# Kernel tuning notes

Measured on AMD Instinct MI355X. Metric: run time of the kernel, lower is better.

The kernel has to match this reference:

```python
import jax, jax.numpy as jnp
import numpy as np

NUM_EDGE_CLASS = 4
NODE_DIM = 64
BATCH = 32
NUM_NODES = 1024


def setup_inputs() -> dict:
    key = jax.random.key(0)
    k1, k2, k3, k4, k5 = jax.random.split(key, 5)
    node_state = jax.random.normal(k1, (BATCH, NUM_NODES, NODE_DIM), dtype=jnp.float32)
    adj_mat = jax.random.randint(k2, (BATCH, NUM_NODES, NUM_NODES), 0, NUM_EDGE_CLASS, dtype=jnp.int32)
    matrix_in = jax.random.normal(k3, (NUM_EDGE_CLASS, NODE_DIM, NODE_DIM), dtype=jnp.float32) * 0.1
    matrix_out = jax.random.normal(k4, (NUM_EDGE_CLASS, NODE_DIM, NODE_DIM), dtype=jnp.float32) * 0.1
    bias = jax.random.normal(k5, (2 * NODE_DIM,), dtype=jnp.float32)
    return {"node_state": node_state, "adj_mat": adj_mat,
            "matrix_in": matrix_in, "matrix_out": matrix_out, "bias": bias}


def reference(node_state, adj_mat, matrix_in, matrix_out, bias):
    """GGNN message passing (Li et al. Eq. 2).

    Original TF code builds a [b, n*d, n*d] block matrix where block (i, j)
    is matrix_in[adj_mat[b, i, j]] (and matrix_out[adj_mat[b, j, i]] for the
    outgoing direction), then matmuls against flattened node states. The
    equivalent fused math is:
      m_in[b,i]  = sum_j matrix_in[adj[b,i,j]]  @ h[b,j]
      m_out[b,i] = sum_j matrix_out[adj[b,j,i]] @ h[b,j]
    Implemented via a one-hot over the (small) set of edge classes so the
    per-edge d x d matrices are never materialized per edge.
    """
    h = node_state  # [b, n, d]
    onehot = jax.nn.one_hot(adj_mat, NUM_EDGE_CLASS, dtype=h.dtype)  # [b, n, n, c]
    # per-class neighbor aggregation, then one small matmul per class
    s_in = jnp.einsum('bijc,bje->bice', onehot, h)          # [b, n, c, d]
    m_in = jnp.einsum('bice,cde->bid', s_in, matrix_in)      # [b, n, d]
    s_out = jnp.einsum('bjic,bje->bice', onehot, h)          # transposed adjacency
    m_out = jnp.einsum('bice,cde->bid', s_out, matrix_out)   # [b, n, d]
    message = jnp.concatenate([m_in, m_out], axis=-1) + bias  # [b, n, 2d]
    return message
```

## Files before the change

### kernel.cpp

```cpp
#include <hip/hip_runtime.h>


namespace {

typedef unsigned int  u32;
typedef unsigned short u16;
typedef __attribute__((ext_vector_type(8))) short bf16x8;
typedef __attribute__((ext_vector_type(4))) float f32x4;

constexpr int NN = 1024;
constexpr int ND = 64;

__device__ inline u16 f2bf(float x) {
    u32 u = __float_as_uint(x);
    return (u16)((u + 0x7FFFu + ((u >> 16) & 1u)) >> 16);
}
__device__ inline float bf2f(u16 x) { return __uint_as_float(((u32)x) << 16); }

__device__ inline u32 oh2(u32 z) {
    return ((z & 1u) | ((z & 4u) << 14)) * 0x3F80u;
}

__global__ __launch_bounds__(256) void pack_adj(
    const int* __restrict__ adj, u32* __restrict__ adjP, u32* __restrict__ adjPT)
{
    __shared__ u32 rp[64][16];
    const int t = threadIdx.x;
    const int bid = blockIdx.x;
    const int b = bid >> 6, It = (bid >> 4) & 3, Jt = (bid >> 2) & 3, s = bid & 3;
    const int* base = adj + ((size_t)b << 20) + (size_t)(It * 256 + s * 64) * NN + Jt * 256;

    const int row = t >> 2, seg = t & 3;
    const int* rptr = base + (size_t)row * NN + seg * 64;
    u32 w[4];
    #pragma unroll
    for (int q = 0; q < 4; ++q) {
        int4 v0 = *(const int4*)(rptr + q * 16 + 0);
        int4 v1 = *(const int4*)(rptr + q * 16 + 4);
        int4 v2 = *(const int4*)(rptr + q * 16 + 8);
        int4 v3 = *(const int4*)(rptr + q * 16 + 12);
        u32 u = (u32)(v0.x & 3) | ((u32)(v0.y & 3) << 2) | ((u32)(v0.z & 3) << 4) | ((u32)(v0.w & 3) << 6)
              | ((u32)(v1.x & 3) << 8) | ((u32)(v1.y & 3) << 10) | ((u32)(v1.z & 3) << 12) | ((u32)(v1.w & 3) << 14)
              | ((u32)(v2.x & 3) << 16) | ((u32)(v2.y & 3) << 18) | ((u32)(v2.z & 3) << 20) | ((u32)(v2.w & 3) << 22)
              | ((u32)(v3.x & 3) << 24) | ((u32)(v3.y & 3) << 26) | ((u32)(v3.z & 3) << 28) | ((u32)(v3.w & 3) << 30);
        w[q] = u;
    }
    u32* op = adjP + (((((size_t)b * 4 + Jt) * 16 + It * 4 + s) * 4 + seg) * 64 + row) * 4;
    *(uint4*)op = make_uint4(w[0], w[1], w[2], w[3]);
    *(uint4*)&rp[row][seg * 4] = make_uint4(w[0], w[1], w[2], w[3]);
    __syncthreads();

    const int sc = t >> 6, il = t & 63;
    const int cw = sc * 4 + (il >> 4);
    const int bp = (il & 15) * 2;
    u32 o[4];
    #pragma unroll
    for (int jj = 0; jj < 4; ++jj) {
        u32 acc = 0;
        #pragma unroll
        for (int k = 0; k < 16; ++k)
            acc |= ((rp[jj * 16 + k][cw] >> bp) & 3u) << (2 * k);
        o[jj] = acc;
    }
    u32* op2 = adjPT + (((((size_t)b * 4 + It) * 16 + Jt * 4 + sc) * 4 + s) * 64 + il) * 4;
    *(uint4*)op2 = make_uint4(o[0], o[1], o[2], o[3]);
}

__global__ __launch_bounds__(256) void prep_h(
    const float* __restrict__ h, u16* __restrict__ Hws, float* __restrict__ PA)
{
    __shared__ u16 hl[256][72];
    const int t = threadIdx.x;
    const int b = blockIdx.x >> 2, jc = blockIdx.x & 3;
    const float* hb = h + ((size_t)b * NN + jc * 256) * ND;
    #pragma unroll
    for (int k = 0; k < 16; ++k) {
        int j = k * 16 + (t >> 4);
        int e4 = (t & 15) * 4;
        float4 v = *(const float4*)(hb + (size_t)j * ND + e4);
        *(u32*)&hl[j][e4]     = (u32)f2bf(v.x) | ((u32)f2bf(v.y) << 16);
        *(u32*)&hl[j][e4 + 2] = (u32)f2bf(v.z) | ((u32)f2bf(v.w) << 16);
    }
    __syncthreads();
    u16* ob = Hws + (size_t)(b * 4 + jc) * 2048 * 8;
    const int e = t & 63;
    float psum = 0.f;
    #pragma unroll
    for (int k = 0; k < 8; ++k) {
        int u = k * 4 + (t >> 6);
        u16 x0 = hl[u * 8 + 0][e], x1 = hl[u * 8 + 1][e], x2 = hl[u * 8 + 2][e], x3 = hl[u * 8 + 3][e];
        u16 x4 = hl[u * 8 + 4][e], x5 = hl[u * 8 + 5][e], x6 = hl[u * 8 + 6][e], x7 = hl[u * 8 + 7][e];
        psum += bf2f(x0) + bf2f(x1) + bf2f(x2) + bf2f(x3) + bf2f(x4) + bf2f(x5) + bf2f(x6) + bf2f(x7);
        u32 p0 = (u32)x0 | ((u32)x1 << 16), p1 = (u32)x2 | ((u32)x3 << 16);
        u32 p2 = (u32)x4 | ((u32)x5 << 16), p3 = (u32)x6 | ((u32)x7 << 16);
        *(uint4*)(ob + (size_t)(u * 64 + e) * 8) = make_uint4(p0, p1, p2, p3);
    }
    atomicAdd(&PA[b * 64 + e], psum);
}

__global__ __launch_bounds__(256) void prep_m(
    const float* __restrict__ Min, const float* __restrict__ Mout,
    const float* __restrict__ bias, const float* __restrict__ PA,
    u16* __restrict__ Mws, float* __restrict__ basews)
{
    const int t = threadIdx.x, bb = blockIdx.x;
    if (bb == 0) {
        for (int i = t; i < 2 * 4096; i += 256) {
            const float* M = (i < 4096) ? Min : Mout;
            int idx = i & 4095;
            float m0 = M[idx], m1 = M[4096 + idx], m2 = M[8192 + idx], m3 = M[12288 + idx];
            u16* o = Mws + (size_t)(i >> 12) * 3 * 4096;
            o[idx]        = f2bf(m1 - m0);
            o[4096 + idx] = f2bf(m2 - m0);
            o[8192 + idx] = f2bf(m0 - m1 - m2 + m3);
        }
    }
    if (t < 128) {
        int d = t & 63, dir = t >> 6;
        const float* M0 = (dir ? Mout : Min) + d * 64;
        float s = bias[dir * 64 + d];
        #pragma unroll 8
        for (int e = 0; e < 64; ++e) s += PA[bb * 64 + e] * M0[e];
        basews[(bb * 2 + dir) * 64 + d] = s;
    }
}

__global__ __launch_bounds__(256) void ggnn_main(
    const u32* __restrict__ adjP, const u32* __restrict__ adjPT,
    const u16* __restrict__ Hws, const u16* __restrict__ Mws,
    const float* __restrict__ basews, float* __restrict__ out)
{
    __shared__ u16 Sb[12][16][72];

    const int t = threadIdx.x;
    const int w = t >> 6;
    const int ln = t & 15, qd = (t & 63) >> 4, qd2 = qd >> 1;
    const int shamt = (qd & 1) * 16;
    const int bid = blockIdx.x;
    const int dir = bid >> 9;
    const int b = (bid >> 4) & 31, it = bid & 15;

    const u32* Adir = dir ? adjPT : adjP;
    f32x4 acc[3][4];
    #pragma unroll
    for (int p = 0; p < 3; ++p)
        #pragma unroll
        for (int nt = 0; nt < 4; ++nt) acc[p][nt] = (f32x4){0.f, 0.f, 0.f, 0.f};

    for (int jc = 0; jc < 4; ++jc) {
        const u32* at = Adir + (size_t)((b * 4 + jc) * 16 + it) * 1024;
        const u16* ht = Hws + (size_t)(b * 4 + jc) * 16384;

        uint4 Ar[4];
        #pragma unroll
        for (int u = 0; u < 4; ++u)
            Ar[u] = *(const uint4*)(at + (u * 64 + w * 16 + ln) * 4);

        #pragma unroll
        for (int ks = 0; ks < 8; ++ks) {
            bf16x8 bf[4];
            #pragma unroll
            for (int nt = 0; nt < 4; ++nt)
                bf[nt] = *(const bf16x8*)(ht + (size_t)((ks * 4 + qd) * 64 + nt * 16 + ln) * 8);

            uint4 Q = Ar[ks >> 1];
            u32 a = (ks & 1) ? (qd2 ? Q.w : Q.z) : (qd2 ? Q.y : Q.x);
            u32 f = (a >> shamt) & 0xFFFFu;
            u32 x0 = f & 0x5555u;
            u32 x1 = (f >> 1) & 0x5555u;
            u32 xt = x0 & x1;

            union { u32 u[4]; bf16x8 v; } A0, A1, AT;
            #pragma unroll
            for (int wd = 0; wd < 4; ++wd) {
                A0.u[wd] = oh2(x0 >> (4 * wd));
                A1.u[wd] = oh2(x1 >> (4 * wd));
                AT.u[wd] = oh2(xt >> (4 * wd));
            }
            #pragma unroll
            for (int nt = 0; nt < 4; ++nt) {
                acc[0][nt] = __builtin_amdgcn_mfma_f32_16x16x32_bf16(A0.v, bf[nt], acc[0][nt], 0, 0, 0);
                acc[1][nt] = __builtin_amdgcn_mfma_f32_16x16x32_bf16(A1.v, bf[nt], acc[1][nt], 0, 0, 0);
                acc[2][nt] = __builtin_amdgcn_mfma_f32_16x16x32_bf16(AT.v, bf[nt], acc[2][nt], 0, 0, 0);
            }
        }
    }

    #pragma unroll
    for (int p = 0; p < 3; ++p)
        #pragma unroll
        for (int nt = 0; nt < 4; ++nt)
            #pragma unroll
            for (int r = 0; r < 4; ++r)
                Sb[w * 3 + p][qd * 4 + r][nt * 16 + ln] = f2bf(acc[p][nt][r]);

    const float* bv = basews + (b * 2 + dir) * 64;
    f32x4 acc2[4];
    #pragma unroll
    for (int dt = 0; dt < 4; ++dt) {
        float v = bv[dt * 16 + ln];
        acc2[dt] = (f32x4){v, v, v, v};
    }
    const u16* Mb = Mws + (size_t)dir * 3 * 4096;
    #pragma unroll
    for (int p = 0; p < 3; ++p) {
        #pragma unroll
        for (int ks2 = 0; ks2 < 2; ++ks2) {
            bf16x8 af = *(const bf16x8*)&Sb[w * 3 + p][ln][ks2 * 32 + qd * 8];
            #pragma unroll
            for (int dt = 0; dt < 4; ++dt) {
                bf16x8 mf = *(const bf16x8*)(Mb + (size_t)(p * 64 + dt * 16 + ln) * 64
                                             + ks2 * 32 + qd * 8);
                acc2[dt] = __builtin_amdgcn_mfma_f32_16x16x32_bf16(af, mf, acc2[dt], 0, 0, 0);
            }
        }
    }
    #pragma unroll
    for (int dt = 0; dt < 4; ++dt)
        #pragma unroll
        for (int r = 0; r < 4; ++r)
            out[((size_t)b * NN + it * 64 + w * 16 + qd * 4 + r) * 128
                + dir * 64 + dt * 16 + ln] = acc2[dt][r];
}

}

extern "C" void kernel_launch(void* const* d_in, const int* in_sizes, int n_in,
                              void* d_out, int out_size, void* d_ws, size_t ws_size,
                              hipStream_t stream) {
    (void)in_sizes; (void)n_in; (void)out_size; (void)ws_size;
    const float* h    = (const float*)d_in[0];
    const int*   adj  = (const int*)d_in[1];
    const float* Min  = (const float*)d_in[2];
    const float* Mout = (const float*)d_in[3];
    const float* bias = (const float*)d_in[4];
    float* out = (float*)d_out;

    char* ws = (char*)d_ws;
    u32* adjP   = (u32*)(ws + 0);
    u32* adjPT  = (u32*)(ws + 8388608);
    u16* Hws    = (u16*)(ws + 16777216);
    float* PA   = (float*)(ws + 20971520);
    u16* Mws    = (u16*)(ws + 20979712);
    float* basews = (float*)(ws + 21028864);

    hipMemsetAsync(PA, 0, 32 * 64 * sizeof(float), stream);
    pack_adj<<<2048, 256, 0, stream>>>(adj, adjP, adjPT);
    prep_h<<<128, 256, 0, stream>>>(h, Hws, PA);
    prep_m<<<32, 256, 0, stream>>>(Min, Mout, bias, PA, Mws, basews);
    ggnn_main<<<1024, 256, 0, stream>>>(adjP, adjPT, Hws, Mws, basews, out);
}
```

Before: 270.4 us.

## Fold matrix prep and base term into main kernel, drop memset and atomics

Merges the matrix-difference prep into an extra block of the adjacency packing kernel. The per-batch column-sum times M0 base term becomes a fourth MFMA pass inside the main kernel, which removes the prep_m launch, the memset and the atomics in prep_h. The transpose in pack_adj now uses a transposed, padded shared layout read with vector loads, and the main kernel prefetches the next adjacency tile into registers under a 4-wave occupancy hint. The cost is extra MFMA and LDS work per block in the main kernel, and rounding the base term to bf16, which lowers its precision.

```diff
diff --git a/kernel.cpp b/kernel.cpp
--- a/kernel.cpp
+++ b/kernel.cpp
@@ -21,12 +21,28 @@
     return ((z & 1u) | ((z & 4u) << 14)) * 0x3F80u;
 }
 
-__global__ __launch_bounds__(256) void pack_adj(
-    const int* __restrict__ adj, u32* __restrict__ adjP, u32* __restrict__ adjPT)
+__global__ __launch_bounds__(256) void pack_adjm(
+    const int* __restrict__ adj, const float* __restrict__ Min,
+    const float* __restrict__ Mout, u32* __restrict__ adjP,
+    u32* __restrict__ adjPT, u16* __restrict__ Mws)
 {
-    __shared__ u32 rp[64][16];
     const int t = threadIdx.x;
     const int bid = blockIdx.x;
+    if (bid >= 2048) {
+        for (int i = t; i < 8192; i += 256) {
+            const float* M = (i < 4096) ? Min : Mout;
+            int idx = i & 4095;
+            float m0 = M[idx], m1 = M[4096 + idx], m2 = M[8192 + idx], m3 = M[12288 + idx];
+            u16* o = Mws + (size_t)(i >> 12) * 16384;
+            o[idx]         = f2bf(m1 - m0);
+            o[4096 + idx]  = f2bf(m2 - m0);
+            o[8192 + idx]  = f2bf(m0 - m1 - m2 + m3);
+            o[12288 + idx] = f2bf(m0);
+        }
+        return;
+    }
+
+    __shared__ u32 rp2[16][68];
     const int b = bid >> 6, It = (bid >> 4) & 3, Jt = (bid >> 2) & 3, s = bid & 3;
     const int* base = adj + ((size_t)b << 20) + (size_t)(It * 256 + s * 64) * NN + Jt * 256;
 
@@ -44,10 +60,10 @@
               | ((u32)(v2.x & 3) << 16) | ((u32)(v2.y & 3) << 18) | ((u32)(v2.z & 3) << 20) | ((u32)(v2.w & 3) << 22)
               | ((u32)(v3.x & 3) << 24) | ((u32)(v3.y & 3) << 26) | ((u32)(v3.z & 3) << 28) | ((u32)(v3.w & 3) << 30);
         w[q] = u;
+        rp2[seg * 4 + q][row] = u;
     }
     u32* op = adjP + (((((size_t)b * 4 + Jt) * 16 + It * 4 + s) * 4 + seg) * 64 + row) * 4;
     *(uint4*)op = make_uint4(w[0], w[1], w[2], w[3]);
-    *(uint4*)&rp[row][seg * 4] = make_uint4(w[0], w[1], w[2], w[3]);
     __syncthreads();
 
     const int sc = t >> 6, il = t & 63;
@@ -56,10 +72,15 @@
     u32 o[4];
     #pragma unroll
     for (int jj = 0; jj < 4; ++jj) {
+        u32 r[16];
+        *(uint4*)&r[0]  = *(const uint4*)&rp2[cw][jj * 16 + 0];
+        *(uint4*)&r[4]  = *(const uint4*)&rp2[cw][jj * 16 + 4];
+        *(uint4*)&r[8]  = *(const uint4*)&rp2[cw][jj * 16 + 8];
+        *(uint4*)&r[12] = *(const uint4*)&rp2[cw][jj * 16 + 12];
         u32 acc = 0;
         #pragma unroll
         for (int k = 0; k < 16; ++k)
-            acc |= ((rp[jj * 16 + k][cw] >> bp) & 3u) << (2 * k);
+            acc += ((r[k] >> bp) & 3u) << (2 * k);
         o[jj] = acc;
     }
     u32* op2 = adjPT + (((((size_t)b * 4 + It) * 16 + Jt * 4 + sc) * 4 + s) * 64 + il) * 4;
@@ -67,9 +88,10 @@
 }
 
 __global__ __launch_bounds__(256) void prep_h(
-    const float* __restrict__ h, u16* __restrict__ Hws, float* __restrict__ PA)
+    const float* __restrict__ h, u16* __restrict__ Hws, float* __restrict__ PApart)
 {
     __shared__ u16 hl[256][72];
+    __shared__ float red[4][64];
     const int t = threadIdx.x;
     const int b = blockIdx.x >> 2, jc = blockIdx.x & 3;
     const float* hb = h + ((size_t)b * NN + jc * 256) * ND;
@@ -95,42 +117,21 @@
         u32 p2 = (u32)x4 | ((u32)x5 << 16), p3 = (u32)x6 | ((u32)x7 << 16);
         *(uint4*)(ob + (size_t)(u * 64 + e) * 8) = make_uint4(p0, p1, p2, p3);
     }
-    atomicAdd(&PA[b * 64 + e], psum);
-}
-
-__global__ __launch_bounds__(256) void prep_m(
-    const float* __restrict__ Min, const float* __restrict__ Mout,
-    const float* __restrict__ bias, const float* __restrict__ PA,
-    u16* __restrict__ Mws, float* __restrict__ basews)
-{
-    const int t = threadIdx.x, bb = blockIdx.x;
-    if (bb == 0) {
-        for (int i = t; i < 2 * 4096; i += 256) {
-            const float* M = (i < 4096) ? Min : Mout;
-            int idx = i & 4095;
-            float m0 = M[idx], m1 = M[4096 + idx], m2 = M[8192 + idx], m3 = M[12288 + idx];
-            u16* o = Mws + (size_t)(i >> 12) * 3 * 4096;
-            o[idx]        = f2bf(m1 - m0);
-            o[4096 + idx] = f2bf(m2 - m0);
-            o[8192 + idx] = f2bf(m0 - m1 - m2 + m3);
-        }
-    }
-    if (t < 128) {
-        int d = t & 63, dir = t >> 6;
-        const float* M0 = (dir ? Mout : Min) + d * 64;
-        float s = bias[dir * 64 + d];
-        #pragma unroll 8
-        for (int e = 0; e < 64; ++e) s += PA[bb * 64 + e] * M0[e];
-        basews[(bb * 2 + dir) * 64 + d] = s;
-    }
-}
-
-__global__ __launch_bounds__(256) void ggnn_main(
+    red[t >> 6][e] = psum;
+    __syncthreads();
+    if (t < 64) {
+        float sum = red[0][t] + red[1][t] + red[2][t] + red[3][t];
+        PApart[(size_t)(jc * 32 + b) * 64 + t] = sum;
+    }
+}
+
+__global__ __launch_bounds__(256, 4) void ggnn_main(
     const u32* __restrict__ adjP, const u32* __restrict__ adjPT,
     const u16* __restrict__ Hws, const u16* __restrict__ Mws,
-    const float* __restrict__ basews, float* __restrict__ out)
+    const float* __restrict__ PApart, const float* __restrict__ bias,
+    float* __restrict__ out)
 {
-    __shared__ u16 Sb[12][16][72];
+    __shared__ u16 Sb[16][16][72];
 
     const int t = threadIdx.x;
     const int w = t >> 6;
@@ -147,14 +148,24 @@
         #pragma unroll
         for (int nt = 0; nt < 4; ++nt) acc[p][nt] = (f32x4){0.f, 0.f, 0.f, 0.f};
 
-    for (int jc = 0; jc < 4; ++jc) {
-        const u32* at = Adir + (size_t)((b * 4 + jc) * 16 + it) * 1024;
-        const u16* ht = Hws + (size_t)(b * 4 + jc) * 16384;
-
-        uint4 Ar[4];
+    uint4 Ar[4];
+    {
+        const u32* at = Adir + (size_t)((b * 4 + 0) * 16 + it) * 1024;
         #pragma unroll
         for (int u = 0; u < 4; ++u)
             Ar[u] = *(const uint4*)(at + (u * 64 + w * 16 + ln) * 4);
+    }
+
+    #pragma unroll
+    for (int jc = 0; jc < 4; ++jc) {
+        const u16* ht = Hws + (size_t)(b * 4 + jc) * 16384;
+        uint4 ArN[4];
+        if (jc < 3) {
+            const u32* at = Adir + (size_t)((b * 4 + jc + 1) * 16 + it) * 1024;
+            #pragma unroll
+            for (int u = 0; u < 4; ++u)
+                ArN[u] = *(const uint4*)(at + (u * 64 + w * 16 + ln) * 4);
+        }
 
         #pragma unroll
         for (int ks = 0; ks < 8; ++ks) {
@@ -184,6 +195,10 @@
                 acc[2][nt] = __builtin_amdgcn_mfma_f32_16x16x32_bf16(AT.v, bf[nt], acc[2][nt], 0, 0, 0);
             }
         }
+        if (jc < 3) {
+            #pragma unroll
+            for (int u = 0; u < 4; ++u) Ar[u] = ArN[u];
+        }
     }
 
     #pragma unroll
@@ -192,21 +207,33 @@
         for (int nt = 0; nt < 4; ++nt)
             #pragma unroll
             for (int r = 0; r < 4; ++r)
-                Sb[w * 3 + p][qd * 4 + r][nt * 16 + ln] = f2bf(acc[p][nt][r]);
-
-    const float* bv = basews + (b * 2 + dir) * 64;
+                Sb[w * 4 + p][qd * 4 + r][nt * 16 + ln] = f2bf(acc[p][nt][r]);
+
+    {
+        const int lane64 = t & 63;
+        float paf = 0.f;
+        #pragma unroll
+        for (int jcp = 0; jcp < 4; ++jcp)
+            paf += PApart[(size_t)(jcp * 32 + b) * 64 + lane64];
+        u16 pab = f2bf(paf);
+        #pragma unroll
+        for (int i = 0; i < 16; ++i)
+            Sb[w * 4 + 3][i][lane64] = pab;
+    }
+
+    const int dofs = dir * 64;
     f32x4 acc2[4];
     #pragma unroll
     for (int dt = 0; dt < 4; ++dt) {
-        float v = bv[dt * 16 + ln];
+        float v = bias[dofs + dt * 16 + ln];
         acc2[dt] = (f32x4){v, v, v, v};
     }
-    const u16* Mb = Mws + (size_t)dir * 3 * 4096;
-    #pragma unroll
-    for (int p = 0; p < 3; ++p) {
+    const u16* Mb = Mws + (size_t)dir * 16384;
+    #pragma unroll
+    for (int p = 0; p < 4; ++p) {
         #pragma unroll
         for (int ks2 = 0; ks2 < 2; ++ks2) {
-            bf16x8 af = *(const bf16x8*)&Sb[w * 3 + p][ln][ks2 * 32 + qd * 8];
+            bf16x8 af = *(const bf16x8*)&Sb[w * 4 + p][ln][ks2 * 32 + qd * 8];
             #pragma unroll
             for (int dt = 0; dt < 4; ++dt) {
                 bf16x8 mf = *(const bf16x8*)(Mb + (size_t)(p * 64 + dt * 16 + ln) * 64
@@ -220,7 +247,7 @@
         #pragma unroll
         for (int r = 0; r < 4; ++r)
             out[((size_t)b * NN + it * 64 + w * 16 + qd * 4 + r) * 128
-                + dir * 64 + dt * 16 + ln] = acc2[dt][r];
+                + dofs + dt * 16 + ln] = acc2[dt][r];
 }
 
 }
@@ -237,16 +264,13 @@
     float* out = (float*)d_out;
 
     char* ws = (char*)d_ws;
-    u32* adjP   = (u32*)(ws + 0);
-    u32* adjPT  = (u32*)(ws + 8388608);
-    u16* Hws    = (u16*)(ws + 16777216);
-    float* PA   = (float*)(ws + 20971520);
-    u16* Mws    = (u16*)(ws + 20979712);
-    float* basews = (float*)(ws + 21028864);
-
-    hipMemsetAsync(PA, 0, 32 * 64 * sizeof(float), stream);
-    pack_adj<<<2048, 256, 0, stream>>>(adj, adjP, adjPT);
-    prep_h<<<128, 256, 0, stream>>>(h, Hws, PA);
-    prep_m<<<32, 256, 0, stream>>>(Min, Mout, bias, PA, Mws, basews);
-    ggnn_main<<<1024, 256, 0, stream>>>(adjP, adjPT, Hws, Mws, basews, out);
-}
+    u32* adjP     = (u32*)(ws + 0);
+    u32* adjPT    = (u32*)(ws + 8388608);
+    u16* Hws      = (u16*)(ws + 16777216);
+    float* PApart = (float*)(ws + 20971520);
+    u16* Mws      = (u16*)(ws + 21004288);
+
+    pack_adjm<<<2049, 256, 0, stream>>>(adj, Min, Mout, adjP, adjPT, Mws);
+    prep_h<<<128, 256, 0, stream>>>(h, Hws, PApart);
+    ggnn_main<<<1024, 256, 0, stream>>>(adjP, adjPT, Hws, Mws, PApart, bias, out);
+}
```

Result: slower. 276.9 us (+2.4%).
